# Kernel tuning notes

Measured on AMD Instinct MI355X. Metric: run time of the kernel, lower is better.

The kernel has to match this reference:

```python
import jax, jax.numpy as jnp
import numpy as np
from functools import partial

V, E, H, HD, OUT = 50000, 256, 512, 256, 2
B, T = 64, 512

def setup_inputs() -> dict:
    key = jax.random.key(0)
    ks = jax.random.split(key, 32)
    def lin(kw, kb, out_d, in_d):
        s = 1.0 / np.sqrt(in_d)
        return (jax.random.uniform(kw, (out_d, in_d), jnp.float32, -s, s),
                jax.random.uniform(kb, (out_d,), jnp.float32, -s, s))
    Wir, bir = lin(ks[0], ks[1], H, E)
    Whr, bhr = lin(ks[2], ks[3], H, H)
    Wif, bif = lin(ks[4], ks[5], H, E)
    Whf, bhf = lin(ks[6], ks[7], H, H)
    Wig, big = lin(ks[8], ks[9], H, E)
    Whg, bhg = lin(ks[10], ks[11], H, H)
    Wio, bio = lin(ks[12], ks[13], H, E)
    Who, bho = lin(ks[14], ks[15], H, H)
    W_ol, b_ol = lin(ks[16], ks[17], HD, H)          # fc_out_lstm
    W_fc, b_fc = lin(ks[18], ks[19], OUT, H + HD)    # fc_out_attent
    emb = jax.random.normal(ks[20], (V, E), jnp.float32)
    W_att = jax.random.normal(ks[21], (HD, H), jnp.float32) * 0.02  # torch init is zeros; use small random so attention is non-trivial
    b_att = jnp.zeros((H,), jnp.float32)
    input_words = jax.random.randint(ks[22], (B, T), 0, V, dtype=jnp.int64)
    return dict(input_words=input_words, emb=emb,
                Wir=Wir, bir=bir, Whr=Whr, bhr=bhr,
                Wif=Wif, bif=bif, Whf=Whf, bhf=bhf,
                Wig=Wig, big=big, Whg=Whg, bhg=bhg,
                Wio=Wio, bio=bio, Who=Who, bho=bho,
                W_att=W_att, b_att=b_att, W_ol=W_ol, b_ol=b_ol,
                W_fc=W_fc, b_fc=b_fc)

def reference(input_words, emb, Wir, bir, Whr, bhr, Wif, bif, Whf, bhf,
              Wig, big, Whg, bhg, Wio, bio, Who, bho,
              W_att, b_att, W_ol, b_ol, W_fc, b_fc):
    b, t = input_words.shape
    h0 = jnp.zeros((b, Whr.shape[0]), emb.dtype)
    c0 = jnp.zeros_like(h0)
    x = emb[input_words].transpose(1, 0, 2)  # [T,B,E]
    # Precompute all input projections as big GEMMs (same math, fused over time)
    pr = jnp.einsum('tbe,he->tbh', x, Wir) + bir
    pf = jnp.einsum('tbe,he->tbh', x, Wif) + bif
    pg = jnp.einsum('tbe,he->tbh', x, Wig) + big
    po = jnp.einsum('tbe,he->tbh', x, Wio) + bio
    def step(carry, pres):
        h, c = carry
        xr, xf, xg, xo = pres
        rt = jax.nn.sigmoid(xr + h @ Whr.T + bhr)
        ft = jax.nn.sigmoid(xf + h @ Whf.T + bhf)
        gt = jnp.tanh(xg + h @ Whg.T + bhg)
        ot = jax.nn.sigmoid(xo + h @ Who.T + bho)
        c = ft * c + rt * gt
        h = ot * jnp.tanh(c)
        return (h, c), h
    (h_last, _), hs = jax.lax.scan(step, (h0, c0), (pr, pf, pg, po))
    final_hidden = h_last @ W_ol.T + b_ol                 # [B,HD]
    outputs = hs.transpose(1, 2, 0)                       # [B,H,T]
    score = final_hidden @ W_att + b_att                  # [B,H]
    att_score = jnp.einsum('bh,bht->bt', score, outputs)  # [B,T]
    dist = jax.nn.softmax(att_score, axis=-1)
    att_out = jnp.einsum('bht,bt->bh', outputs, dist)     # [B,H]
    out = jnp.concatenate([final_hidden, att_out], axis=1) @ W_fc.T + b_fc
    return jax.nn.sigmoid(out), h_last
```

## Files before the change

### kernel.cpp

```cpp
#include <hip/hip_runtime.h>
#include <cstdint>
#include <cstddef>

typedef unsigned short u16;
typedef unsigned int u32;
typedef unsigned long long u64;
typedef __attribute__((ext_vector_type(8))) short bfrag8;
typedef __attribute__((ext_vector_type(4))) float f32x4;

#define NB 64
#define NT 512
#define NE 256
#define NH 512
#define NWGW 128
#define NBLK 256
#define WSTR 408

__device__ __forceinline__ float bf2f(u16 b) { return __uint_as_float(((unsigned)b) << 16); }
__device__ __forceinline__ u16 f2bf(float f) {
  unsigned u = __float_as_uint(f);
  u += 0x7fffu + ((u >> 16) & 1u);
  return (u16)(u >> 16);
}
__device__ __forceinline__ float fsigm(float x) { return 1.0f / (1.0f + __expf(-x)); }
__device__ __forceinline__ float ftanh(float x) { return 2.0f / (1.0f + __expf(-2.0f * x)) - 1.0f; }

__device__ __forceinline__ void split1(float v, u16& h, u16& l) {
  h = f2bf(v);
  float r = v - bf2f(h);
  l = f2bf(r);
}
__device__ __forceinline__ void split8(const float* p, bfrag8& hi, bfrag8& lo) {
#pragma unroll
  for (int i = 0; i < 8; ++i) {
    u16 h, l; split1(p[i], h, l);
    hi[i] = (short)h; lo[i] = (short)l;
  }
}

__device__ __forceinline__ void unpack8(uint4 q, float* o) {
  o[0] = __uint_as_float(q.x << 16); o[1] = __uint_as_float(q.x & 0xffff0000u);
  o[2] = __uint_as_float(q.y << 16); o[3] = __uint_as_float(q.y & 0xffff0000u);
  o[4] = __uint_as_float(q.z << 16); o[5] = __uint_as_float(q.z & 0xffff0000u);
  o[6] = __uint_as_float(q.w << 16); o[7] = __uint_as_float(q.w & 0xffff0000u);
}

__global__ __launch_bounds__(64) void stage_weights(
    const float* __restrict__ Whr, const float* __restrict__ Whf,
    const float* __restrict__ Whg, const float* __restrict__ Who,
    const float* __restrict__ Wir, const float* __restrict__ Wif,
    const float* __restrict__ Wig, const float* __restrict__ Wio,
    const float* __restrict__ bhr, const float* __restrict__ bhf,
    const float* __restrict__ bhg, const float* __restrict__ bho,
    const float* __restrict__ bir, const float* __restrict__ bif,
    const float* __restrict__ big_, const float* __restrict__ bio,
    u16* __restrict__ wbuf, float* __restrict__ bias_s)
{
  const int wg = blockIdx.x;
  const int lane = threadIdx.x;
  const int colq = lane & 15;
  const int koff = (lane >> 4) * 8;
  const int gate = colq >> 2;
  const int gu = wg * 4 + (colq & 3);
  const float* wh = (gate == 0) ? Whr : (gate == 1) ? Whf : (gate == 2) ? Whg : Who;
  const float* wi = (gate == 0) ? Wir : (gate == 1) ? Wif : (gate == 2) ? Wig : Wio;
  u16* wb = wbuf + (size_t)(wg * 64 + lane) * 48 * 8;
  const float* whp = wh + (size_t)gu * NH + koff;
  const float* wip = wi + (size_t)gu * NE + koff;
#pragma unroll
  for (int kt = 0; kt < 16; ++kt) {
    bfrag8 hi, lo; split8(whp + kt * 32, hi, lo);
    *(bfrag8*)(wb + kt * 8) = hi;
    *(bfrag8*)(wb + (16 + kt) * 8) = lo;
  }
#pragma unroll
  for (int kt = 0; kt < 8; ++kt) {
    bfrag8 hi, lo; split8(wip + kt * 32, hi, lo);
    *(bfrag8*)(wb + (32 + kt) * 8) = hi;
    *(bfrag8*)(wb + (40 + kt) * 8) = lo;
  }
  if (lane < 16) {
    int g2 = lane >> 2, u2 = lane & 3, gu2 = wg * 4 + u2;
    const float* bh = (g2 == 0) ? bhr : (g2 == 1) ? bhf : (g2 == 2) ? bhg : bho;
    const float* bi = (g2 == 0) ? bir : (g2 == 1) ? bif : (g2 == 2) ? big_ : bio;
    bias_s[wg * 16 + lane] = bh[gu2] + bi[gu2];
  }
}

__global__ __launch_bounds__(256, 1) void lstm_persist(
    const int* __restrict__ words,
    const float* __restrict__ emb,
    const u16* __restrict__ wbuf,
    const float* __restrict__ bias_s,
    u64* __restrict__ hbuf,
    u16* __restrict__ hs_all,
    float* __restrict__ hlast,
    u32* __restrict__ slots)
{
  const int G    = blockIdx.x >> 6;
  const int ib   = blockIdx.x & 63;
  const int tid  = threadIdx.x;
  const int lane = tid & 63;
  const int wave = tid >> 6;
  const int colq = lane & 15;
  const int koff = (lane >> 4) * 8;
  const int arow = 16 * G + colq;

  __shared__ u16 wlds[2 * 64 * WSTR];
  __shared__ float pl[4 * 16 * 34];
  __shared__ float biasLds[32];

  if (wave < 2) {
    const u16* src = wbuf + (size_t)((ib * 2 + wave) * 64 + lane) * 384;
    u16* dst = wlds + (size_t)(wave * 64 + lane) * WSTR;
#pragma unroll
    for (int i = 0; i < 48; ++i)
      *(bfrag8*)(dst + i * 8) = *(const bfrag8*)(src + i * 8);
  }
  if (tid < 32) biasLds[tid] = bias_s[ib * 32 + tid];
  __syncthreads();

  const bool is64 = ((words[1] | words[3] | words[5] | words[7]) == 0);
  const int r_loc = tid >> 3;
  const int uo    = tid & 7;
  float creg = 0.0f;

  f32x4 xa[2], xb[2];
  {
    int widx = arow * NT + 0;
    int wd = is64 ? words[2 * widx] : words[widx];
    const float* xs = emb + (size_t)wd * NE + wave * 64 + koff;
    xa[0] = *(const f32x4*)(xs);      xb[0] = *(const f32x4*)(xs + 4);
    xa[1] = *(const f32x4*)(xs + 32); xb[1] = *(const f32x4*)(xs + 36);
  }

  const u16* wl0 = wlds + (size_t)lane * WSTR;
  const u16* wl1 = wlds + (size_t)(64 + lane) * WSTR;
  const size_t pstore = (size_t)G * 4096 + (size_t)(ib >> 4) * 1024
                      + (size_t)((ib >> 2) & 3) * 256 + (size_t)(uo >> 1) * 64
                      + (size_t)((ib & 3) * 16 + r_loc);
  u32* postp = slots + (G * 64 + ib) * 16;
  const u32* pollp = slots + (G * 64 + 16 * wave + colq) * 16;

  for (int t = 1; t <= NT; ++t) {
    const u32 need = (u32)(t - 1);

    u32 pv0 = 0;
    if (t > 1)
      pv0 = __hip_atomic_load(pollp, __ATOMIC_RELAXED, __HIP_MEMORY_SCOPE_AGENT);

    bfrag8 xh[2], xl[2];
#pragma unroll
    for (int xt = 0; xt < 2; ++xt)
#pragma unroll
      for (int i = 0; i < 4; ++i) {
        u16 h, l;
        split1(xa[xt][i], h, l); xh[xt][i] = (short)h;     xl[xt][i] = (short)l;
        split1(xb[xt][i], h, l); xh[xt][4 + i] = (short)h; xl[xt][4 + i] = (short)l;
      }

    f32x4 acc0 = {0.f, 0.f, 0.f, 0.f};
    f32x4 acc1 = {0.f, 0.f, 0.f, 0.f};

#pragma unroll
    for (int xt = 0; xt < 2; ++xt) {
      int f = 2 * wave + xt;
      bfrag8 wih = *(const bfrag8*)(wl0 + (32 + f) * 8);
      bfrag8 wil = *(const bfrag8*)(wl0 + (40 + f) * 8);
      acc0 = __builtin_amdgcn_mfma_f32_16x16x32_bf16(xh[xt], wih, acc0, 0, 0, 0);
      acc0 = __builtin_amdgcn_mfma_f32_16x16x32_bf16(xl[xt], wih, acc0, 0, 0, 0);
      acc0 = __builtin_amdgcn_mfma_f32_16x16x32_bf16(xh[xt], wil, acc0, 0, 0, 0);
    }
#pragma unroll
    for (int xt = 0; xt < 2; ++xt) {
      int f = 2 * wave + xt;
      bfrag8 wih = *(const bfrag8*)(wl1 + (32 + f) * 8);
      bfrag8 wil = *(const bfrag8*)(wl1 + (40 + f) * 8);
      acc1 = __builtin_amdgcn_mfma_f32_16x16x32_bf16(xh[xt], wih, acc1, 0, 0, 0);
      acc1 = __builtin_amdgcn_mfma_f32_16x16x32_bf16(xl[xt], wih, acc1, 0, 0, 0);
      acc1 = __builtin_amdgcn_mfma_f32_16x16x32_bf16(xh[xt], wil, acc1, 0, 0, 0);
    }

    u64 q[16];
    if (t > 1) {
      u32 a = pv0;
      u32 bfl = __hip_atomic_load(pollp, __ATOMIC_RELAXED, __HIP_MEMORY_SCOPE_AGENT);
      while (!__all((int)(a >= need))) {
        a = bfl;
        bfl = __hip_atomic_load(pollp, __ATOMIC_RELAXED, __HIP_MEMORY_SCOPE_AGENT);
      }
      asm volatile("" ::: "memory");

      const u64* hb = hbuf + ((size_t)(((t - 1) & 1) * 16 + G * 4 + wave)) * 1024 + lane;
#pragma unroll
      for (int i = 0; i < 16; ++i)
        q[i] = __hip_atomic_load(hb + (size_t)i * 64, __ATOMIC_RELAXED, __HIP_MEMORY_SCOPE_AGENT);
    }

    if (t < NT) {
      int widx = arow * NT + t;
      int wd = is64 ? words[2 * widx] : words[widx];
      const float* xs = emb + (size_t)wd * NE + wave * 64 + koff;
      xa[0] = *(const f32x4*)(xs);      xb[0] = *(const f32x4*)(xs + 4);
      xa[1] = *(const f32x4*)(xs + 32); xb[1] = *(const f32x4*)(xs + 36);
    }

    if (t > 1) {
#pragma unroll
      for (int ktl = 0; ktl < 4; ++ktl) {
        bfrag8 ah, al;
#pragma unroll
        for (int p = 0; p < 4; ++p) {
          u64 vq = q[ktl * 4 + p];
          u32 w0 = (u32)vq, w1 = (u32)(vq >> 32);
          ah[2 * p]     = (short)(w0 >> 16); al[2 * p]     = (short)(w0 & 0xffffu);
          ah[2 * p + 1] = (short)(w1 >> 16); al[2 * p + 1] = (short)(w1 & 0xffffu);
        }
        int f = 4 * wave + ktl;
        bfrag8 whh0 = *(const bfrag8*)(wl0 + f * 8);
        bfrag8 whl0 = *(const bfrag8*)(wl0 + (16 + f) * 8);
        bfrag8 whh1 = *(const bfrag8*)(wl1 + f * 8);
        bfrag8 whl1 = *(const bfrag8*)(wl1 + (16 + f) * 8);
        acc0 = __builtin_amdgcn_mfma_f32_16x16x32_bf16(ah, whh0, acc0, 0, 0, 0);
        acc1 = __builtin_amdgcn_mfma_f32_16x16x32_bf16(ah, whh1, acc1, 0, 0, 0);
        acc0 = __builtin_amdgcn_mfma_f32_16x16x32_bf16(al, whh0, acc0, 0, 0, 0);
        acc1 = __builtin_amdgcn_mfma_f32_16x16x32_bf16(al, whh1, acc1, 0, 0, 0);
        acc0 = __builtin_amdgcn_mfma_f32_16x16x32_bf16(ah, whl0, acc0, 0, 0, 0);
        acc1 = __builtin_amdgcn_mfma_f32_16x16x32_bf16(ah, whl1, acc1, 0, 0, 0);
      }
    }

    {
      int rb = (lane >> 4) << 2;
#pragma unroll
      for (int r = 0; r < 4; ++r) {
        pl[(wave * 16 + rb + r) * 34 + colq] = acc0[r];
        pl[(wave * 16 + rb + r) * 34 + 16 + colq] = acc1[r];
      }
    }
    __syncthreads();

    if (tid < 128) {
      int clb = ((uo >> 2) << 4) + (uo & 3);
      const float* pr = pl + r_loc * 34;
      float xr = biasLds[clb], xf = biasLds[clb + 4];
      float xg = biasLds[clb + 8], xo = biasLds[clb + 12];
#pragma unroll
      for (int w = 0; w < 4; ++w) {
        const float* pw = pr + w * 16 * 34;
        xr += pw[clb]; xf += pw[clb + 4]; xg += pw[clb + 8]; xo += pw[clb + 12];
      }
      float rg = fsigm(xr), fg = fsigm(xf), gg = ftanh(xg), og = fsigm(xo);
      creg = fg * creg + rg * gg;
      float hv = og * ftanh(creg);
      u16 hhi, hlo; split1(hv, hhi, hlo);
      u32 hval = ((u32)hhi << 16) | (u32)hlo;
      u32 pv = (u32)__shfl_xor((int)hval, 1);
      int grow = 16 * G + r_loc;
      int gcol = 8 * ib + uo;
      if ((uo & 1) == 0) {
        u64 e = (u64)hval | ((u64)pv << 32);
        __hip_atomic_store(hbuf + (size_t)(t & 1) * 16384 + pstore, e,
                           __ATOMIC_RELAXED, __HIP_MEMORY_SCOPE_AGENT);
        u32 hspack = (u32)hhi | (pv & 0xffff0000u);
        *(u32*)&hs_all[(size_t)(t - 1) * (NB * NH) + (size_t)grow * NH + gcol] = hspack;
      }
      if (t == NT) hlast[grow * NH + gcol] = hv;
    }

    __syncthreads();
    if (tid == 0)
      __hip_atomic_store(postp, (u32)t, __ATOMIC_RELAXED, __HIP_MEMORY_SCOPE_AGENT);
  }
}

__global__ __launch_bounds__(256) void post_kernel(
    const float* __restrict__ hlast,
    const u16* __restrict__ hs,
    const float* __restrict__ W_ol, const float* __restrict__ b_ol,
    const float* __restrict__ W_att, const float* __restrict__ b_att,
    const float* __restrict__ W_fc, const float* __restrict__ b_fc,
    float* __restrict__ out)
{
  int b = blockIdx.x, tid = threadIdx.x;
  __shared__ float hl[NH], fh[256], sc[NH], att[NT], ao[NH], red[256];
  __shared__ u16 rowbuf[16 * 520];

  for (int i = tid; i < NH; i += 256) {
    float hv = hlast[b * NH + i];
    hl[i] = hv;
    out[128 + b * NH + i] = hv;
  }
  __syncthreads();

  {
    float s = b_ol[tid];
    const float* w = W_ol + (size_t)tid * NH;
    for (int k = 0; k < NH; k += 4) {
      f32x4 q = *(const f32x4*)(w + k);
      s += q[0] * hl[k] + q[1] * hl[k + 1] + q[2] * hl[k + 2] + q[3] * hl[k + 3];
    }
    fh[tid] = s;
  }
  __syncthreads();

  for (int h = tid; h < NH; h += 256) {
    float s = b_att[h];
    for (int j = 0; j < 256; ++j) s += fh[j] * W_att[(size_t)j * NH + h];
    sc[h] = s;
  }
  __syncthreads();

  {
    int r = tid >> 4, p = tid & 15;
    for (int t0 = 0; t0 < NT; t0 += 16) {
      const u16* src = hs + ((size_t)(t0 + r) * NB + b) * NH + p * 32;
      uint4 v0 = *(const uint4*)(src);
      uint4 v1 = *(const uint4*)(src + 8);
      uint4 v2 = *(const uint4*)(src + 16);
      uint4 v3 = *(const uint4*)(src + 24);
      u16* dst = rowbuf + r * 520 + p * 32;
      *(uint4*)(dst) = v0; *(uint4*)(dst + 8) = v1;
      *(uint4*)(dst + 16) = v2; *(uint4*)(dst + 24) = v3;
      __syncthreads();
      const u16* row = rowbuf + r * 520 + p * 32;
      float s = 0.f;
      for (int k = 0; k < 32; k += 8) {
        uint4 qv = *(const uint4*)(row + k);
        float tmp[8]; unpack8(qv, tmp);
        const float* scv = &sc[p * 32 + k];
#pragma unroll
        for (int j = 0; j < 8; ++j) s += tmp[j] * scv[j];
      }
      s += __shfl_xor(s, 1); s += __shfl_xor(s, 2);
      s += __shfl_xor(s, 4); s += __shfl_xor(s, 8);
      if (p == 0) att[t0 + r] = s;
      __syncthreads();
    }
  }

  float l0 = att[tid], l1 = att[tid + 256];
  red[tid] = fmaxf(l0, l1);
  __syncthreads();
  for (int s = 128; s > 0; s >>= 1) { if (tid < s) red[tid] = fmaxf(red[tid], red[tid + s]); __syncthreads(); }
  float mx = red[0];
  __syncthreads();
  float e0 = __expf(l0 - mx), e1 = __expf(l1 - mx);
  red[tid] = e0 + e1;
  __syncthreads();
  for (int s = 128; s > 0; s >>= 1) { if (tid < s) red[tid] += red[tid + s]; __syncthreads(); }
  float inv = 1.0f / red[0];
  __syncthreads();
  att[tid] = e0 * inv;
  att[tid + 256] = e1 * inv;
  __syncthreads();

  {
    float a0 = 0.f, a1 = 0.f;
    for (int t = 0; t < NT; ++t) {
      float d = att[t];
      const u16* row = hs + ((size_t)t * NB + b) * NH;
      a0 += d * bf2f(row[tid]);
      a1 += d * bf2f(row[tid + 256]);
    }
    ao[tid] = a0;
    ao[tid + 256] = a1;
  }
  __syncthreads();

#pragma unroll
  for (int o = 0; o < 2; ++o) {
    float part = 0.f;
    for (int i = tid; i < 768; i += 256) {
      float v = (i < 256) ? fh[i] : ao[i - 256];
      part += v * W_fc[o * 768 + i];
    }
    red[tid] = part;
    __syncthreads();
    for (int s = 128; s > 0; s >>= 1) { if (tid < s) red[tid] += red[tid + s]; __syncthreads(); }
    if (tid == 0) out[b * 2 + o] = fsigm(red[0] + b_fc[o]);
    __syncthreads();
  }
}

extern "C" void kernel_launch(void* const* d_in, const int* in_sizes, int n_in,
                              void* d_out, int out_size, void* d_ws, size_t ws_size,
                              hipStream_t stream) {
  const int* words  = (const int*)d_in[0];
  const float* emb  = (const float*)d_in[1];
  const float* Wir  = (const float*)d_in[2];  const float* bir = (const float*)d_in[3];
  const float* Whr  = (const float*)d_in[4];  const float* bhr = (const float*)d_in[5];
  const float* Wif  = (const float*)d_in[6];  const float* bif = (const float*)d_in[7];
  const float* Whf  = (const float*)d_in[8];  const float* bhf = (const float*)d_in[9];
  const float* Wig  = (const float*)d_in[10]; const float* big_ = (const float*)d_in[11];
  const float* Whg  = (const float*)d_in[12]; const float* bhg = (const float*)d_in[13];
  const float* Wio  = (const float*)d_in[14]; const float* bio = (const float*)d_in[15];
  const float* Who  = (const float*)d_in[16]; const float* bho = (const float*)d_in[17];
  const float* W_att = (const float*)d_in[18]; const float* b_att = (const float*)d_in[19];
  const float* W_ol  = (const float*)d_in[20]; const float* b_ol  = (const float*)d_in[21];
  const float* W_fc  = (const float*)d_in[22]; const float* b_fc  = (const float*)d_in[23];

  uint8_t* ws = (uint8_t*)d_ws;
  u16* hs       = (u16*)ws;
  size_t off    = (size_t)33554432;
  u16* wbuf     = (u16*)(ws + off);   off += 6291456;
  float* bias_s = (float*)(ws + off); off += 8192;
  u64* hbuf     = (u64*)(ws + off);   off += 262144;
  float* hlast  = (float*)(ws + off); off += 131072;
  u32* slots    = (u32*)(ws + off);

  hipMemsetAsync(slots, 0, 16384, stream);

  stage_weights<<<dim3(NWGW), dim3(64), 0, stream>>>(
      Whr, Whf, Whg, Who, Wir, Wif, Wig, Wio,
      bhr, bhf, bhg, bho, bir, bif, big_, bio, wbuf, bias_s);

  lstm_persist<<<dim3(NBLK), dim3(256), 0, stream>>>(
      words, emb, wbuf, bias_s, hbuf, hs, hlast, slots);

  post_kernel<<<dim3(NB), dim3(256), 0, stream>>>(hlast, hs, W_ol, b_ol, W_att, b_att,
                                                  W_fc, b_fc, (float*)d_out);
}
```

Before: 1.871 ms.

## Split persistent LSTM across 512 blocks with one weight tile per block

Doubles the persistent grid to 512 blocks with two blocks per CU allowed. Each block now owns one 64-row weight tile (4 hidden units) instead of two, halving its LDS footprint and per-step MFMA work. The hbuf store layout, slot indexing and polling are remapped to match, with each wave now polling 32 producer slots. The simpler poll loop drops the old early prefetch of the flag. This spreads the recurrent step over more CUs and waves, in exchange for more producers to synchronise with each step and higher polling traffic.

```diff
diff --git a/kernel.cpp b/kernel.cpp
--- a/kernel.cpp
+++ b/kernel.cpp
@@ -13,7 +13,7 @@
 #define NE 256
 #define NH 512
 #define NWGW 128
-#define NBLK 256
+#define NBLK 512
 #define WSTR 408
 
 __device__ __forceinline__ float bf2f(u16 b) { return __uint_as_float(((unsigned)b) << 16); }
@@ -87,7 +87,7 @@
   }
 }
 
-__global__ __launch_bounds__(256, 1) void lstm_persist(
+__global__ __launch_bounds__(256, 2) void lstm_persist(
     const int* __restrict__ words,
     const float* __restrict__ emb,
     const u16* __restrict__ wbuf,
@@ -97,8 +97,8 @@
     float* __restrict__ hlast,
     u32* __restrict__ slots)
 {
-  const int G    = blockIdx.x >> 6;
-  const int ib   = blockIdx.x & 63;
+  const int G    = blockIdx.x >> 7;
+  const int ib   = blockIdx.x & 127;
   const int tid  = threadIdx.x;
   const int lane = tid & 63;
   const int wave = tid >> 6;
@@ -106,23 +106,23 @@
   const int koff = (lane >> 4) * 8;
   const int arow = 16 * G + colq;
 
-  __shared__ u16 wlds[2 * 64 * WSTR];
-  __shared__ float pl[4 * 16 * 34];
-  __shared__ float biasLds[32];
-
-  if (wave < 2) {
-    const u16* src = wbuf + (size_t)((ib * 2 + wave) * 64 + lane) * 384;
-    u16* dst = wlds + (size_t)(wave * 64 + lane) * WSTR;
+  __shared__ u16 wlds[64 * WSTR];
+  __shared__ float pl[4 * 16 * 17];
+  __shared__ float biasLds[16];
+
+  if (wave == 0) {
+    const u16* src = wbuf + (size_t)(ib * 64 + lane) * 384;
+    u16* dst = wlds + (size_t)lane * WSTR;
 #pragma unroll
     for (int i = 0; i < 48; ++i)
       *(bfrag8*)(dst + i * 8) = *(const bfrag8*)(src + i * 8);
   }
-  if (tid < 32) biasLds[tid] = bias_s[ib * 32 + tid];
+  if (tid < 16) biasLds[tid] = bias_s[ib * 16 + tid];
   __syncthreads();
 
   const bool is64 = ((words[1] | words[3] | words[5] | words[7]) == 0);
-  const int r_loc = tid >> 3;
-  const int uo    = tid & 7;
+  const int r_loc = (tid >> 2) & 15;
+  const int uo    = tid & 3;
   float creg = 0.0f;
 
   f32x4 xa[2], xb[2];
@@ -134,21 +134,15 @@
     xa[1] = *(const f32x4*)(xs + 32); xb[1] = *(const f32x4*)(xs + 36);
   }
 
-  const u16* wl0 = wlds + (size_t)lane * WSTR;
-  const u16* wl1 = wlds + (size_t)(64 + lane) * WSTR;
-  const size_t pstore = (size_t)G * 4096 + (size_t)(ib >> 4) * 1024
-                      + (size_t)((ib >> 2) & 3) * 256 + (size_t)(uo >> 1) * 64
-                      + (size_t)((ib & 3) * 16 + r_loc);
-  u32* postp = slots + (G * 64 + ib) * 16;
-  const u32* pollp = slots + (G * 64 + 16 * wave + colq) * 16;
+  const u16* wl = wlds + (size_t)lane * WSTR;
+  const size_t pstore = (size_t)G * 4096 + (size_t)(ib >> 5) * 1024
+                      + (size_t)((ib >> 3) & 3) * 256
+                      + (size_t)(2 * (ib & 1) + (uo >> 1)) * 64
+                      + (size_t)(((ib >> 1) & 3) * 16 + r_loc);
+  u32* postp = slots + (G * 128 + ib) * 16;
+  const u32* pollp = slots + (G * 128 + 32 * wave + (lane & 31)) * 16;
 
   for (int t = 1; t <= NT; ++t) {
-    const u32 need = (u32)(t - 1);
-
-    u32 pv0 = 0;
-    if (t > 1)
-      pv0 = __hip_atomic_load(pollp, __ATOMIC_RELAXED, __HIP_MEMORY_SCOPE_AGENT);
-
     bfrag8 xh[2], xl[2];
 #pragma unroll
     for (int xt = 0; xt < 2; ++xt)
@@ -158,44 +152,6 @@
         split1(xa[xt][i], h, l); xh[xt][i] = (short)h;     xl[xt][i] = (short)l;
         split1(xb[xt][i], h, l); xh[xt][4 + i] = (short)h; xl[xt][4 + i] = (short)l;
       }
-
-    f32x4 acc0 = {0.f, 0.f, 0.f, 0.f};
-    f32x4 acc1 = {0.f, 0.f, 0.f, 0.f};
-
-#pragma unroll
-    for (int xt = 0; xt < 2; ++xt) {
-      int f = 2 * wave + xt;
-      bfrag8 wih = *(const bfrag8*)(wl0 + (32 + f) * 8);
-      bfrag8 wil = *(const bfrag8*)(wl0 + (40 + f) * 8);
-      acc0 = __builtin_amdgcn_mfma_f32_16x16x32_bf16(xh[xt], wih, acc0, 0, 0, 0);
-      acc0 = __builtin_amdgcn_mfma_f32_16x16x32_bf16(xl[xt], wih, acc0, 0, 0, 0);
-      acc0 = __builtin_amdgcn_mfma_f32_16x16x32_bf16(xh[xt], wil, acc0, 0, 0, 0);
-    }
-#pragma unroll
-    for (int xt = 0; xt < 2; ++xt) {
-      int f = 2 * wave + xt;
-      bfrag8 wih = *(const bfrag8*)(wl1 + (32 + f) * 8);
-      bfrag8 wil = *(const bfrag8*)(wl1 + (40 + f) * 8);
-      acc1 = __builtin_amdgcn_mfma_f32_16x16x32_bf16(xh[xt], wih, acc1, 0, 0, 0);
-      acc1 = __builtin_amdgcn_mfma_f32_16x16x32_bf16(xl[xt], wih, acc1, 0, 0, 0);
-      acc1 = __builtin_amdgcn_mfma_f32_16x16x32_bf16(xh[xt], wil, acc1, 0, 0, 0);
-    }
-
-    u64 q[16];
-    if (t > 1) {
-      u32 a = pv0;
-      u32 bfl = __hip_atomic_load(pollp, __ATOMIC_RELAXED, __HIP_MEMORY_SCOPE_AGENT);
-      while (!__all((int)(a >= need))) {
-        a = bfl;
-        bfl = __hip_atomic_load(pollp, __ATOMIC_RELAXED, __HIP_MEMORY_SCOPE_AGENT);
-      }
-      asm volatile("" ::: "memory");
-
-      const u64* hb = hbuf + ((size_t)(((t - 1) & 1) * 16 + G * 4 + wave)) * 1024 + lane;
-#pragma unroll
-      for (int i = 0; i < 16; ++i)
-        q[i] = __hip_atomic_load(hb + (size_t)i * 64, __ATOMIC_RELAXED, __HIP_MEMORY_SCOPE_AGENT);
-    }
 
     if (t < NT) {
       int widx = arow * NT + t;
@@ -205,7 +161,32 @@
       xa[1] = *(const f32x4*)(xs + 32); xb[1] = *(const f32x4*)(xs + 36);
     }
 
+    f32x4 acc = {0.f, 0.f, 0.f, 0.f};
+
+#pragma unroll
+    for (int xt = 0; xt < 2; ++xt) {
+      int f = 2 * wave + xt;
+      bfrag8 wih = *(const bfrag8*)(wl + (32 + f) * 8);
+      bfrag8 wil = *(const bfrag8*)(wl + (40 + f) * 8);
+      acc = __builtin_amdgcn_mfma_f32_16x16x32_bf16(xh[xt], wih, acc, 0, 0, 0);
+      acc = __builtin_amdgcn_mfma_f32_16x16x32_bf16(xl[xt], wih, acc, 0, 0, 0);
+      acc = __builtin_amdgcn_mfma_f32_16x16x32_bf16(xh[xt], wil, acc, 0, 0, 0);
+    }
+
     if (t > 1) {
+      const u32 need = (u32)(t - 1);
+      u32 v;
+      do {
+        v = __hip_atomic_load(pollp, __ATOMIC_RELAXED, __HIP_MEMORY_SCOPE_AGENT);
+      } while (!__all((int)(v >= need)));
+      asm volatile("" ::: "memory");
+
+      const u64* hb = hbuf + ((size_t)(((t - 1) & 1) * 16 + G * 4 + wave)) * 1024 + lane;
+      u64 q[16];
+#pragma unroll
+      for (int i = 0; i < 16; ++i)
+        q[i] = __hip_atomic_load(hb + (size_t)i * 64, __ATOMIC_RELAXED, __HIP_MEMORY_SCOPE_AGENT);
+
 #pragma unroll
       for (int ktl = 0; ktl < 4; ++ktl) {
         bfrag8 ah, al;
@@ -217,38 +198,30 @@
           ah[2 * p + 1] = (short)(w1 >> 16); al[2 * p + 1] = (short)(w1 & 0xffffu);
         }
         int f = 4 * wave + ktl;
-        bfrag8 whh0 = *(const bfrag8*)(wl0 + f * 8);
-        bfrag8 whl0 = *(const bfrag8*)(wl0 + (16 + f) * 8);
-        bfrag8 whh1 = *(const bfrag8*)(wl1 + f * 8);
-        bfrag8 whl1 = *(const bfrag8*)(wl1 + (16 + f) * 8);
-        acc0 = __builtin_amdgcn_mfma_f32_16x16x32_bf16(ah, whh0, acc0, 0, 0, 0);
-        acc1 = __builtin_amdgcn_mfma_f32_16x16x32_bf16(ah, whh1, acc1, 0, 0, 0);
-        acc0 = __builtin_amdgcn_mfma_f32_16x16x32_bf16(al, whh0, acc0, 0, 0, 0);
-        acc1 = __builtin_amdgcn_mfma_f32_16x16x32_bf16(al, whh1, acc1, 0, 0, 0);
-        acc0 = __builtin_amdgcn_mfma_f32_16x16x32_bf16(ah, whl0, acc0, 0, 0, 0);
-        acc1 = __builtin_amdgcn_mfma_f32_16x16x32_bf16(ah, whl1, acc1, 0, 0, 0);
+        bfrag8 whh = *(const bfrag8*)(wl + f * 8);
+        bfrag8 whl = *(const bfrag8*)(wl + (16 + f) * 8);
+        acc = __builtin_amdgcn_mfma_f32_16x16x32_bf16(ah, whh, acc, 0, 0, 0);
+        acc = __builtin_amdgcn_mfma_f32_16x16x32_bf16(al, whh, acc, 0, 0, 0);
+        acc = __builtin_amdgcn_mfma_f32_16x16x32_bf16(ah, whl, acc, 0, 0, 0);
       }
     }
 
     {
       int rb = (lane >> 4) << 2;
 #pragma unroll
-      for (int r = 0; r < 4; ++r) {
-        pl[(wave * 16 + rb + r) * 34 + colq] = acc0[r];
-        pl[(wave * 16 + rb + r) * 34 + 16 + colq] = acc1[r];
-      }
+      for (int r = 0; r < 4; ++r)
+        pl[(wave * 16 + rb + r) * 17 + colq] = acc[r];
     }
     __syncthreads();
 
-    if (tid < 128) {
-      int clb = ((uo >> 2) << 4) + (uo & 3);
-      const float* pr = pl + r_loc * 34;
-      float xr = biasLds[clb], xf = biasLds[clb + 4];
-      float xg = biasLds[clb + 8], xo = biasLds[clb + 12];
+    if (tid < 64) {
+      const float* pr = pl + r_loc * 17;
+      float xr = biasLds[uo], xf = biasLds[uo + 4];
+      float xg = biasLds[uo + 8], xo = biasLds[uo + 12];
 #pragma unroll
       for (int w = 0; w < 4; ++w) {
-        const float* pw = pr + w * 16 * 34;
-        xr += pw[clb]; xf += pw[clb + 4]; xg += pw[clb + 8]; xo += pw[clb + 12];
+        const float* pw = pr + w * 16 * 17;
+        xr += pw[uo]; xf += pw[4 + uo]; xg += pw[8 + uo]; xo += pw[12 + uo];
       }
       float rg = fsigm(xr), fg = fsigm(xf), gg = ftanh(xg), og = fsigm(xo);
       creg = fg * creg + rg * gg;
@@ -257,7 +230,7 @@
       u32 hval = ((u32)hhi << 16) | (u32)hlo;
       u32 pv = (u32)__shfl_xor((int)hval, 1);
       int grow = 16 * G + r_loc;
-      int gcol = 8 * ib + uo;
+      int gcol = 4 * ib + uo;
       if ((uo & 1) == 0) {
         u64 e = (u64)hval | ((u64)pv << 32);
         __hip_atomic_store(hbuf + (size_t)(t & 1) * 16384 + pstore, e,
@@ -409,7 +382,7 @@
   float* hlast  = (float*)(ws + off); off += 131072;
   u32* slots    = (u32*)(ws + off);
 
-  hipMemsetAsync(slots, 0, 16384, stream);
+  hipMemsetAsync(slots, 0, 32768, stream);
 
   stage_weights<<<dim3(NWGW), dim3(64), 0, stream>>>(
       Whr, Whf, Whg, Who, Wir, Wif, Wig, Wio,
```

After: 1.829 ms. 1.02x faster.
